# Performance work log

Measured on AMD Instinct MI355X. Metric: run time of the kernel, lower is better.

Reference implementation:

```python
import jax, jax.numpy as jnp
import numpy as np


def setup_inputs() -> dict:
    key = jax.random.key(0)
    k1, k2 = jax.random.split(key)
    N, B, E, H = 2048, 8, 256, 512
    x = jax.random.normal(k1, (N, B, E), dtype=jnp.float32)
    h = jax.random.normal(k2, (N, B, H), dtype=jnp.float32)
    return {"x": x, "h": h}


def reference(x, h):
    # x: (N, B, E), h: (N, B, H)
    H = h.shape[-1]
    xt = jnp.transpose(x, (1, 0, 2))            # (B, N, E)
    norm = jnp.linalg.norm(xt, axis=2, keepdims=True)  # (B, N, 1)
    xn = xt / norm
    # cosine-similarity scores, softmax over keys (last dim)
    scores = jax.nn.softmax(jnp.einsum('bie,bje->bij', xn, xn), axis=2)  # (B, N, N)
    ht = jnp.transpose(h, (1, 0, 2))            # (B, N, H)
    # The original expands scores/h over an H-fold dim, bmm's, and sums;
    # that equals H * (scores @ h). Keep the H factor for faithfulness
    # (it cancels in the global-norm division below).
    g = H * jnp.einsum('bij,bjh->bih', scores, ht)  # (B, N, H)
    g = jnp.transpose(g, (1, 0, 2))             # (N, B, H)
    return g / jnp.linalg.norm(g)
```

## Files before the change

### kernel.cpp

```cpp
#include <hip/hip_runtime.h>

#define N_TOK 2048
#define B_SZ  8
#define E_DIM 256
#define H_DIM 512
#define ITERS (N_TOK / 32)

typedef __attribute__((ext_vector_type(8))) short bf16x8;
typedef __attribute__((ext_vector_type(4))) float f32x4;
typedef __attribute__((ext_vector_type(4))) unsigned short u16x4;

__device__ __forceinline__ unsigned short f2bf(float f) {
    union { float f; unsigned u; } v; v.f = f;
    unsigned r = v.u + 0x7FFF + ((v.u >> 16) & 1);
    return (unsigned short)(r >> 16);
}
__device__ __forceinline__ float bf2f(unsigned short b) {
    union { unsigned u; float f; } v; v.u = ((unsigned)b) << 16;
    return v.f;
}

__global__ void prep_kernel(const float* __restrict__ x,
                            const float* __restrict__ hptr,
                            unsigned short* __restrict__ Xn,
                            unsigned short* __restrict__ Vp,
                            float* __restrict__ sumsq) {
    int bid = blockIdx.x;
    int t = threadIdx.x;
    if (bid == 0 && t == 0) *sumsq = 0.0f;
    if (bid < (N_TOK * B_SZ) / 4) {
        int w = t >> 6, lane = t & 63;
        int r = bid * 4 + w;
        int n = r >> 3, b = r & 7;
        float4 v = *(const float4*)(x + (size_t)r * E_DIM + lane * 4);
        float s = v.x * v.x + v.y * v.y + v.z * v.z + v.w * v.w;
        #pragma unroll
        for (int o = 32; o > 0; o >>= 1) s += __shfl_xor(s, o);
        float rn = 1.0f / sqrtf(s);
        u16x4 pk;
        pk[0] = f2bf(v.x * rn); pk[1] = f2bf(v.y * rn);
        pk[2] = f2bf(v.z * rn); pk[3] = f2bf(v.w * rn);
        int u = lane >> 1, half = lane & 1;
        *(u16x4*)(Xn + ((size_t)b * N_TOK + n) * E_DIM
                     + (size_t)((u ^ (n & 7)) * 8 + half * 4)) = pk;
    } else {
        int lin = bid - (N_TOK * B_SZ) / 4;
        int jb = lin & 63, hb = (lin >> 6) & 15, b = lin >> 10;
        __shared__ __attribute__((aligned(16))) float tile[32][36];
        int j0 = jb * 32, h0 = hb * 32;
        {
            int j = t >> 3, c = (t & 7) * 4;
            float4 v = *(const float4*)(hptr +
                ((size_t)(j0 + j) * B_SZ + b) * H_DIM + h0 + c);
            *(float4*)(&tile[j][c]) = v;
        }
        __syncthreads();
        size_t base = ((size_t)b * (N_TOK / 32) + jb) * (H_DIM * 32);
        int hcl = t >> 3, jg = (t >> 1) & 3, half = t & 1;
        int hc = h0 + hcl;
        u16x4 pk;
        #pragma unroll
        for (int k = 0; k < 4; k++)
            pk[k] = f2bf(tile[jg * 8 + half * 4 + k][hcl]);
        *(u16x4*)(Vp + base + (size_t)(hc * 4 + (jg ^ ((hcl >> 1) & 3))) * 8
                     + half * 4) = pk;
    }
}

#define PT_STRIDE 40

__launch_bounds__(256, 2)
__global__ void flash_kernel(const unsigned short* __restrict__ Xn,
                             const unsigned short* __restrict__ Vp,
                             float* __restrict__ out,
                             float* __restrict__ sumsq) {
    __shared__ __attribute__((aligned(16))) unsigned short Kbuf[2][32 * 256];
    __shared__ __attribute__((aligned(16))) unsigned short Pt[2][16 * PT_STRIDE];
    __shared__ float Lred[2][2][16];

    int b  = blockIdx.x;
    int q0 = blockIdx.y * 32;
    int t = threadIdx.x;
    int w = t >> 6, lane = t & 63;
    int quad = lane >> 4, nm = lane & 15;
    int rg = w >> 1, kh = w & 1;

    const unsigned short* Kbase = Xn + (size_t)b * N_TOK * E_DIM;
    const unsigned short* Qrow =
        Xn + ((size_t)b * N_TOK + q0 + rg * 16 + nm) * E_DIM;
    const unsigned short* Vtile0 = Vp + (size_t)b * (N_TOK / 32) * (H_DIM * 32);

    bf16x8 qf[8];
    #pragma unroll
    for (int ec = 0; ec < 8; ec++)
        qf[ec] = *(const bf16x8*)(Qrow + (size_t)(((ec * 4 + quad) ^ (nm & 7)) * 8));

    f32x4 O[16];
    #pragma unroll
    for (int i = 0; i < 16; i++) O[i] = (f32x4){0.f, 0.f, 0.f, 0.f};
    float l_lane[4];
    #pragma unroll
    for (int r = 0; r < 4; r++) l_lane[r] = 0.0f;

    auto stage = [&](int tile, int buf) {
        const unsigned short* src0 = Kbase + (size_t)tile * 32 * E_DIM;
        #pragma unroll
        for (int k = 0; k < 4; k++) {
            int chunk = w * 4 + k;
            __builtin_amdgcn_global_load_lds(
                (const __attribute__((address_space(1))) unsigned int*)
                    (src0 + (size_t)chunk * 512 + lane * 8),
                (__attribute__((address_space(3))) unsigned int*)
                    (&Kbuf[buf][chunk * 512]),
                16, 0, 0);
        }
    };

    stage(0, 0);
    int vswz = (quad ^ ((nm >> 1) & 3)) * 8;
    int krow = kh * 16 + nm;

    for (int it = 0; it < ITERS; ++it) {
        __syncthreads();
        int cur = it & 1;

        const unsigned short* Vt = Vtile0 + (size_t)it * (H_DIM * 32);
        bf16x8 vf[16];
        #pragma unroll
        for (int tt = 0; tt < 16; tt++) {
            int hc = kh * 256 + tt * 16 + nm;
            vf[tt] = *(const bf16x8*)(Vt + (size_t)(hc * 4) * 8 + vswz);
        }

        if (it + 1 < ITERS) stage(it + 1, cur ^ 1);
        const unsigned short* KB = &Kbuf[cur][0];

        f32x4 sa = (f32x4){0.f,0.f,0.f,0.f}, sb = (f32x4){0.f,0.f,0.f,0.f};
        #pragma unroll
        for (int ec = 0; ec < 4; ec++) {
            int u0 = (((2*ec)   * 4 + quad) ^ (nm & 7)) * 8;
            int u1 = (((2*ec+1) * 4 + quad) ^ (nm & 7)) * 8;
            bf16x8 kf0 = *(const bf16x8*)(KB + krow * 256 + u0);
            bf16x8 kf1 = *(const bf16x8*)(KB + krow * 256 + u1);
            sa = __builtin_amdgcn_mfma_f32_16x16x32_bf16(qf[2*ec],   kf0, sa, 0, 0, 0);
            sb = __builtin_amdgcn_mfma_f32_16x16x32_bf16(qf[2*ec+1], kf1, sb, 0, 0, 0);
        }

        #pragma unroll
        for (int r = 0; r < 4; r++) {
            unsigned short pb = f2bf(__expf((sa[r] + sb[r]) - 1.0f));
            l_lane[r] += bf2f(pb);
            Pt[rg][(quad * 4 + r) * PT_STRIDE + kh * 16 + nm] = pb;
        }

        asm volatile("s_waitcnt lgkmcnt(0)" ::: "memory");
        __builtin_amdgcn_s_barrier();
        asm volatile("" ::: "memory");

        bf16x8 pf = *(const bf16x8*)(&Pt[rg][nm * PT_STRIDE + quad * 8]);

        #pragma unroll
        for (int tt = 0; tt < 16; tt++)
            O[tt] = __builtin_amdgcn_mfma_f32_16x16x32_bf16(pf, vf[tt], O[tt], 0, 0, 0);
    }

    float lv[4];
    #pragma unroll
    for (int r = 0; r < 4; r++) {
        float v = l_lane[r];
        #pragma unroll
        for (int o = 1; o < 16; o <<= 1) v += __shfl_xor(v, o);
        lv[r] = v;
    }
    if (nm == 0) {
        #pragma unroll
        for (int r = 0; r < 4; r++) Lred[rg][kh][quad * 4 + r] = lv[r];
    }
    __syncthreads();
    float linv[4];
    #pragma unroll
    for (int r = 0; r < 4; r++)
        linv[r] = 1.0f / (Lred[rg][0][quad * 4 + r] + Lred[rg][1][quad * 4 + r]);

    float ss = 0.0f;
    #pragma unroll
    for (int tt = 0; tt < 16; tt++) {
        #pragma unroll
        for (int r = 0; r < 4; r++) {
            float val = O[tt][r] * linv[r];
            int row = q0 + rg * 16 + quad * 4 + r;
            int col = kh * 256 + tt * 16 + nm;
            out[((size_t)row * B_SZ + b) * H_DIM + col] = val;
            ss += val * val;
        }
    }
    #pragma unroll
    for (int o = 1; o < 64; o <<= 1) ss += __shfl_xor(ss, o);
    if (lane == 0) atomicAdd(sumsq, ss);
}

__global__ void scale_kernel(float* __restrict__ out,
                             const float* __restrict__ sumsq) {
    size_t idx = ((size_t)blockIdx.x * blockDim.x + threadIdx.x) * 4;
    float rs = 1.0f / sqrtf(*sumsq);
    float4 v = *(float4*)(out + idx);
    v.x *= rs; v.y *= rs; v.z *= rs; v.w *= rs;
    *(float4*)(out + idx) = v;
}

extern "C" void kernel_launch(void* const* d_in, const int* in_sizes, int n_in,
                              void* d_out, int out_size, void* d_ws, size_t ws_size,
                              hipStream_t stream) {
    const float* x = (const float*)d_in[0];
    const float* h = (const float*)d_in[1];
    float* out = (float*)d_out;

    unsigned short* Xn = (unsigned short*)d_ws;
    unsigned short* Vp = Xn + (size_t)B_SZ * N_TOK * E_DIM;
    float* sumsq = (float*)(Vp + (size_t)B_SZ * N_TOK * H_DIM);

    prep_kernel<<<(N_TOK * B_SZ) / 4 + (N_TOK / 32) * (H_DIM / 32) * B_SZ,
                  256, 0, stream>>>(x, h, Xn, Vp, sumsq);
    flash_kernel<<<dim3(B_SZ, N_TOK / 32), 256, 0, stream>>>(Xn, Vp, out, sumsq);
    scale_kernel<<<out_size / (4 * 256), 256, 0, stream>>>(out, sumsq);
}
```

Baseline: 221.4 us.

## Retile flash kernel to 64 query rows and split H across grid z

Each block now handles 64 query rows (one 16-row group per wave), and each wave computes full 32-key scores and shares its P tile through LDS so that every wave multiplies all four row groups against its own 64-column H slice. The H dimension is split across two blocks along grid z. This cuts per-wave V fragment loads from 16 to 4 per iteration and reuses each V fragment across 4 row groups, lowering register pressure and global V traffic per output. The cost is that QK^T scores are computed twice, once per z-half, doubling score MFMA and K staging work.

```diff
diff --git a/kernel.cpp b/kernel.cpp
--- a/kernel.cpp
+++ b/kernel.cpp
@@ -5,6 +5,7 @@
 #define E_DIM 256
 #define H_DIM 512
 #define ITERS (N_TOK / 32)
+#define QROWS 64
 
 typedef __attribute__((ext_vector_type(8))) short bf16x8;
 typedef __attribute__((ext_vector_type(4))) float f32x4;
@@ -75,29 +76,32 @@
                              float* __restrict__ out,
                              float* __restrict__ sumsq) {
     __shared__ __attribute__((aligned(16))) unsigned short Kbuf[2][32 * 256];
-    __shared__ __attribute__((aligned(16))) unsigned short Pt[2][16 * PT_STRIDE];
-    __shared__ float Lred[2][2][16];
+    __shared__ __attribute__((aligned(16))) unsigned short Pt[4][16 * PT_STRIDE];
+    __shared__ float Lred[4][16];
 
     int b  = blockIdx.x;
-    int q0 = blockIdx.y * 32;
+    int q0 = blockIdx.y * QROWS;
+    int z  = blockIdx.z;
     int t = threadIdx.x;
     int w = t >> 6, lane = t & 63;
     int quad = lane >> 4, nm = lane & 15;
-    int rg = w >> 1, kh = w & 1;
 
     const unsigned short* Kbase = Xn + (size_t)b * N_TOK * E_DIM;
     const unsigned short* Qrow =
-        Xn + ((size_t)b * N_TOK + q0 + rg * 16 + nm) * E_DIM;
+        Xn + ((size_t)b * N_TOK + q0 + w * 16 + nm) * E_DIM;
     const unsigned short* Vtile0 = Vp + (size_t)b * (N_TOK / 32) * (H_DIM * 32);
+    int col0 = z * 256 + w * 64;
 
     bf16x8 qf[8];
     #pragma unroll
     for (int ec = 0; ec < 8; ec++)
         qf[ec] = *(const bf16x8*)(Qrow + (size_t)(((ec * 4 + quad) ^ (nm & 7)) * 8));
 
-    f32x4 O[16];
-    #pragma unroll
-    for (int i = 0; i < 16; i++) O[i] = (f32x4){0.f, 0.f, 0.f, 0.f};
+    f32x4 O[4][4];
+    #pragma unroll
+    for (int i = 0; i < 4; i++)
+        #pragma unroll
+        for (int j = 0; j < 4; j++) O[i][j] = (f32x4){0.f, 0.f, 0.f, 0.f};
     float l_lane[4];
     #pragma unroll
     for (int r = 0; r < 4; r++) l_lane[r] = 0.0f;
@@ -118,17 +122,16 @@
 
     stage(0, 0);
     int vswz = (quad ^ ((nm >> 1) & 3)) * 8;
-    int krow = kh * 16 + nm;
 
     for (int it = 0; it < ITERS; ++it) {
         __syncthreads();
         int cur = it & 1;
 
         const unsigned short* Vt = Vtile0 + (size_t)it * (H_DIM * 32);
-        bf16x8 vf[16];
-        #pragma unroll
-        for (int tt = 0; tt < 16; tt++) {
-            int hc = kh * 256 + tt * 16 + nm;
+        bf16x8 vf[4];
+        #pragma unroll
+        for (int tt = 0; tt < 4; tt++) {
+            int hc = col0 + tt * 16 + nm;
             vf[tt] = *(const bf16x8*)(Vt + (size_t)(hc * 4) * 8 + vswz);
         }
 
@@ -137,31 +140,35 @@
 
         f32x4 sa = (f32x4){0.f,0.f,0.f,0.f}, sb = (f32x4){0.f,0.f,0.f,0.f};
         #pragma unroll
-        for (int ec = 0; ec < 4; ec++) {
-            int u0 = (((2*ec)   * 4 + quad) ^ (nm & 7)) * 8;
-            int u1 = (((2*ec+1) * 4 + quad) ^ (nm & 7)) * 8;
-            bf16x8 kf0 = *(const bf16x8*)(KB + krow * 256 + u0);
-            bf16x8 kf1 = *(const bf16x8*)(KB + krow * 256 + u1);
-            sa = __builtin_amdgcn_mfma_f32_16x16x32_bf16(qf[2*ec],   kf0, sa, 0, 0, 0);
-            sb = __builtin_amdgcn_mfma_f32_16x16x32_bf16(qf[2*ec+1], kf1, sb, 0, 0, 0);
+        for (int ec = 0; ec < 8; ec++) {
+            int u = ((ec * 4 + quad) ^ (nm & 7)) * 8;
+            bf16x8 kf0 = *(const bf16x8*)(KB + nm * 256 + u);
+            bf16x8 kf1 = *(const bf16x8*)(KB + (16 + nm) * 256 + u);
+            sa = __builtin_amdgcn_mfma_f32_16x16x32_bf16(qf[ec], kf0, sa, 0, 0, 0);
+            sb = __builtin_amdgcn_mfma_f32_16x16x32_bf16(qf[ec], kf1, sb, 0, 0, 0);
         }
 
         #pragma unroll
         for (int r = 0; r < 4; r++) {
-            unsigned short pb = f2bf(__expf((sa[r] + sb[r]) - 1.0f));
-            l_lane[r] += bf2f(pb);
-            Pt[rg][(quad * 4 + r) * PT_STRIDE + kh * 16 + nm] = pb;
+            unsigned short pb0 = f2bf(__expf(sa[r] - 1.0f));
+            unsigned short pb1 = f2bf(__expf(sb[r] - 1.0f));
+            l_lane[r] += bf2f(pb0) + bf2f(pb1);
+            Pt[w][(quad * 4 + r) * PT_STRIDE + nm]      = pb0;
+            Pt[w][(quad * 4 + r) * PT_STRIDE + 16 + nm] = pb1;
         }
 
         asm volatile("s_waitcnt lgkmcnt(0)" ::: "memory");
         __builtin_amdgcn_s_barrier();
         asm volatile("" ::: "memory");
 
-        bf16x8 pf = *(const bf16x8*)(&Pt[rg][nm * PT_STRIDE + quad * 8]);
-
-        #pragma unroll
-        for (int tt = 0; tt < 16; tt++)
-            O[tt] = __builtin_amdgcn_mfma_f32_16x16x32_bf16(pf, vf[tt], O[tt], 0, 0, 0);
+        #pragma unroll
+        for (int rg = 0; rg < 4; rg++) {
+            bf16x8 pf = *(const bf16x8*)(&Pt[rg][nm * PT_STRIDE + quad * 8]);
+            #pragma unroll
+            for (int ct = 0; ct < 4; ct++)
+                O[rg][ct] = __builtin_amdgcn_mfma_f32_16x16x32_bf16(
+                    pf, vf[ct], O[rg][ct], 0, 0, 0);
+        }
     }
 
     float lv[4];
@@ -174,24 +181,27 @@
     }
     if (nm == 0) {
         #pragma unroll
-        for (int r = 0; r < 4; r++) Lred[rg][kh][quad * 4 + r] = lv[r];
+        for (int r = 0; r < 4; r++) Lred[w][quad * 4 + r] = lv[r];
     }
     __syncthreads();
-    float linv[4];
-    #pragma unroll
-    for (int r = 0; r < 4; r++)
-        linv[r] = 1.0f / (Lred[rg][0][quad * 4 + r] + Lred[rg][1][quad * 4 + r]);
 
     float ss = 0.0f;
     #pragma unroll
-    for (int tt = 0; tt < 16; tt++) {
-        #pragma unroll
-        for (int r = 0; r < 4; r++) {
-            float val = O[tt][r] * linv[r];
-            int row = q0 + rg * 16 + quad * 4 + r;
-            int col = kh * 256 + tt * 16 + nm;
-            out[((size_t)row * B_SZ + b) * H_DIM + col] = val;
-            ss += val * val;
+    for (int rg = 0; rg < 4; rg++) {
+        float linv[4];
+        #pragma unroll
+        for (int r = 0; r < 4; r++)
+            linv[r] = 1.0f / Lred[rg][quad * 4 + r];
+        #pragma unroll
+        for (int ct = 0; ct < 4; ct++) {
+            #pragma unroll
+            for (int r = 0; r < 4; r++) {
+                float val = O[rg][ct][r] * linv[r];
+                int row = q0 + rg * 16 + quad * 4 + r;
+                int col = col0 + ct * 16 + nm;
+                out[((size_t)row * B_SZ + b) * H_DIM + col] = val;
+                ss += val * val;
+            }
         }
     }
     #pragma unroll
@@ -221,6 +231,7 @@
 
     prep_kernel<<<(N_TOK * B_SZ) / 4 + (N_TOK / 32) * (H_DIM / 32) * B_SZ,
                   256, 0, stream>>>(x, h, Xn, Vp, sumsq);
-    flash_kernel<<<dim3(B_SZ, N_TOK / 32), 256, 0, stream>>>(Xn, Vp, out, sumsq);
+    flash_kernel<<<dim3(B_SZ, N_TOK / QROWS, 2), 256, 0, stream>>>(
+        Xn, Vp, out, sumsq);
     scale_kernel<<<out_size / (4 * 256), 256, 0, stream>>>(out, sumsq);
 }
```

Result: faster. 206.2 us (-6.9%).
